# Kernel tuning notes

Hardware: AMD Instinct MI355X
Metric: run time of the kernel (lower is better)

The kernel has to match this reference:

```python
import jax, jax.numpy as jnp
import numpy as np

N, E, D = 20000, 320000, 128


def _glorot(key, shape):
    fan_in, fan_out = shape[0], shape[-1]
    lim = jnp.sqrt(6.0 / (fan_in + fan_out)).astype(jnp.float32)
    return jax.random.uniform(key, shape, jnp.float32, -lim, lim)


def setup_inputs() -> dict:
    key = jax.random.key(0)
    ks = jax.random.split(key, 16)
    h = jax.random.normal(ks[0], (N, 1, D), jnp.float32)
    x = jax.random.normal(ks[1], (N, 3), jnp.float32)
    edge_index = jax.random.randint(ks[2], (2, E), 0, N, jnp.int64)
    # edge_mlp: SPDMLP(2D -> D -> D), 2 linear layers with ReLU between
    W1e = _glorot(ks[3], (2 * D, D)); b1e = jnp.zeros((D,), jnp.float32)
    W2e = _glorot(ks[4], (D, D));     b2e = jnp.zeros((D,), jnp.float32)
    # edge_inf: Linear(D, 1) + Sigmoid
    Wg = _glorot(ks[5], (D, 1));      bg = jnp.zeros((1,), jnp.float32)
    # node_mlp: SPDMLP(2D -> D -> D)
    W1n = _glorot(ks[6], (2 * D, D)); b1n = jnp.zeros((D,), jnp.float32)
    W2n = _glorot(ks[7], (D, D));     b2n = jnp.zeros((D,), jnp.float32)
    return {"h": h, "x": x, "edge_index": edge_index,
            "W1e": W1e, "b1e": b1e, "W2e": W2e, "b2e": b2e,
            "Wg": Wg, "bg": bg,
            "W1n": W1n, "b1n": b1n, "W2n": W2n, "b2n": b2n}


def _feature_joint(a, b):
    # a: [B, Na, Da], b: [B, Nb, Db] -> [B, Na+Nb, Da+Db] block-diagonal concat
    Da, Db = a.shape[2], b.shape[2]
    a_exp = jnp.concatenate([a, jnp.zeros(a.shape[:2] + (Db,), a.dtype)], axis=2)
    b_exp = jnp.concatenate([jnp.zeros(b.shape[:2] + (Da,), b.dtype), b], axis=2)
    return jnp.concatenate([a_exp, b_exp], axis=1)


def _mlp2(y, W1, b1, W2, b2):
    return jax.nn.relu(y @ W1 + b1) @ W2 + b2


def reference(h, x, edge_index, W1e, b1e, W2e, b2e, Wg, bg, W1n, b1n, W2n, b2n):
    src, dst = edge_index[0], edge_index[1]
    hi, hj = h[dst], h[src]                              # [E, 1, D] each
    mij = _mlp2(_feature_joint(hi, hj), W1e, b1e, W2e, b2e)  # [E, 2, D]
    eij = jax.nn.sigmoid(mij @ Wg + bg)                  # [E, 2, 1]
    mi = jax.ops.segment_sum(mij * eij, dst, num_segments=h.shape[0])  # [N, 2, D]
    h_new = h + _mlp2(_feature_joint(mi, h), W1n, b1n, W2n, b2n)       # [N, 3, D]
    return (h_new, x)
```

## Files before the change

### kernel.cpp

```cpp
#include <hip/hip_runtime.h>

#define D    128
#define SP   136
#define FS   132
#define NC   2
#define CAP  64

typedef __attribute__((ext_vector_type(8))) short bf16x8;
typedef __attribute__((ext_vector_type(4))) float f32x4;
typedef unsigned short u16;

__device__ __forceinline__ float sigmoidf(float v) { return 1.0f / (1.0f + __expf(-v)); }

__device__ __forceinline__ u16 f2bf(float x) {
    union { float f; unsigned u; } c; c.f = x;
    return (u16)((c.u + 0x7fffu + ((c.u >> 16) & 1u)) >> 16);
}
__device__ __forceinline__ float bflo(unsigned u) {
    union { unsigned v; float f; } c; c.v = u << 16; return c.f;
}
__device__ __forceinline__ float bfhi(unsigned u) {
    union { unsigned v; float f; } c; c.v = u & 0xffff0000u; return c.f;
}
__device__ __forceinline__ void acc8(float* a, uint4 q) {
    a[0] += bflo(q.x); a[1] += bfhi(q.x);
    a[2] += bflo(q.y); a[3] += bfhi(q.y);
    a[4] += bflo(q.z); a[5] += bfhi(q.z);
    a[6] += bflo(q.w); a[7] += bfhi(q.w);
}

__device__ __forceinline__ void layer32(
    const u16* __restrict__ plane, const short* __restrict__ WbM,
    int lane, int ctbase, f32x4 acc[NC][2])
{
    #pragma unroll
    for (int ks = 0; ks < 4; ++ks) {
        bf16x8 a[2];
        #pragma unroll
        for (int rt = 0; rt < 2; ++rt)
            a[rt] = *reinterpret_cast<const bf16x8*>(
                plane + (rt * 16 + (lane & 15)) * SP + ks * 32 + (lane >> 4) * 8);
        #pragma unroll
        for (int c = 0; c < NC; ++c) {
            const bf16x8 b = *reinterpret_cast<const bf16x8*>(
                WbM + ((ctbase + c) * 4 + ks) * 512 + lane * 8);
            #pragma unroll
            for (int rt = 0; rt < 2; ++rt)
                acc[c][rt] = __builtin_amdgcn_mfma_f32_16x16x32_bf16(a[rt], b, acc[c][rt], 0, 0, 0);
        }
    }
}

__device__ __forceinline__ void store_t32(
    const f32x4 acc[NC][2], const float b1v[NC],
    u16* __restrict__ dst, int lane, int ctbase)
{
    #pragma unroll
    for (int c = 0; c < NC; ++c)
        #pragma unroll
        for (int rt = 0; rt < 2; ++rt)
            #pragma unroll
            for (int rr = 0; rr < 4; ++rr)
                dst[(rt * 16 + (lane >> 4) * 4 + rr) * SP + (ctbase + c) * 16 + (lane & 15)] =
                    f2bf(fmaxf(acc[c][rt][rr] + b1v[c], 0.f));
}

__device__ __forceinline__ void stage32(
    const float* __restrict__ src, int base, int N, int tid, u16* __restrict__ plane)
{
    #pragma unroll
    for (int it = 0; it < 4; ++it) {
        const int idx = it * 256 + tid;
        const int row = idx >> 5, c4 = (idx & 31) << 2;
        int node = base + row; if (node >= N) node = N - 1;
        const float4 v = *reinterpret_cast<const float4*>(&src[(size_t)node * D + c4]);
        ushort4 s;
        s.x = f2bf(v.x); s.y = f2bf(v.y); s.z = f2bf(v.z); s.w = f2bf(v.w);
        *reinterpret_cast<ushort4*>(&plane[row * SP + c4]) = s;
    }
}

__device__ __forceinline__ void mlp_tail(
    const short* __restrict__ Wb, int mA,
    const float* __restrict__ b1n, const float* __restrict__ b2n,
    const float* __restrict__ h, float* __restrict__ out_h,
    int r, int base, int N,
    u16* __restrict__ P1, u16* __restrict__ P2, u16* __restrict__ smem)
{
    const int tid = threadIdx.x, lane = tid & 63, w = tid >> 6;
    const int ctbase = w * NC;

    float b1v[NC], b2v[NC];
    #pragma unroll
    for (int c = 0; c < NC; ++c) {
        const int j = (ctbase + c) * 16 + (lane & 15);
        b1v[c] = b1n[j]; b2v[c] = b2n[j];
    }

    f32x4 acc[NC][2];
    #pragma unroll
    for (int c = 0; c < NC; ++c)
        #pragma unroll
        for (int rt = 0; rt < 2; ++rt) acc[c][rt] = (f32x4){0.f, 0.f, 0.f, 0.f};
    layer32(P1, Wb + (size_t)mA * 16384, lane, ctbase, acc);
    store_t32(acc, b1v, P2, lane, ctbase);
    __syncthreads();

    f32x4 o[NC][2];
    #pragma unroll
    for (int c = 0; c < NC; ++c)
        #pragma unroll
        for (int rt = 0; rt < 2; ++rt) o[c][rt] = (f32x4){0.f, 0.f, 0.f, 0.f};
    layer32(P2, Wb + (size_t)5 * 16384, lane, ctbase, o);
    __syncthreads();

    float* fs = reinterpret_cast<float*>(smem);
    #pragma unroll
    for (int c = 0; c < NC; ++c)
        #pragma unroll
        for (int rt = 0; rt < 2; ++rt)
            #pragma unroll
            for (int rr = 0; rr < 4; ++rr)
                fs[(rt * 16 + (lane >> 4) * 4 + rr) * FS + (ctbase + c) * 16 + (lane & 15)] =
                    o[c][rt][rr] + b2v[c];
    __syncthreads();

    const int nl = tid >> 3, cg = tid & 7;
    const int node = base + nl;
    if (node < N) {
        #pragma unroll
        for (int k = 0; k < 4; ++k) {
            float4 ov = *reinterpret_cast<const float4*>(&fs[nl * FS + cg * 16 + k * 4]);
            const float4 hv = *reinterpret_cast<const float4*>(&h[(size_t)node * D + cg * 16 + k * 4]);
            ov.x += hv.x; ov.y += hv.y; ov.z += hv.z; ov.w += hv.w;
            *reinterpret_cast<float4*>(&out_h[((size_t)node * 3 + r) * D + cg * 16 + k * 4]) = ov;
        }
    }
}

__global__ __launch_bounds__(256) void zero_repack_x_kernel(
    int* __restrict__ cnt, int N, int ZB,
    const float* __restrict__ W1e, const float* __restrict__ W2e,
    const float* __restrict__ W1n, const float* __restrict__ W2n,
    short* __restrict__ Wb,
    const float* __restrict__ x, float* __restrict__ out_x)
{
    const int RB = 48;
    if (blockIdx.x < (unsigned)ZB) {
        const int i = blockIdx.x * 256 + threadIdx.x;
        if (i < N) cnt[i] = 0;
        return;
    }
    if (blockIdx.x >= (unsigned)(ZB + RB)) {
        const int i4 = ((blockIdx.x - ZB - RB) * 256 + threadIdx.x) * 4;
        const int total = N * 3;
        if (i4 + 3 < total) {
            *reinterpret_cast<float4*>(&out_x[i4]) =
                *reinterpret_cast<const float4*>(&x[i4]);
        } else {
            for (int k = i4; k < total && k < i4 + 4; ++k) out_x[k] = x[k];
        }
        return;
    }
    const int gid = (blockIdx.x - ZB) * 256 + threadIdx.x;
    if (gid >= 6 * 8 * 4 * 64) return;
    const int lane = gid & 63;
    int t = gid >> 6;
    const int ks = t & 3; t >>= 2;
    const int ct = t & 7;
    const int m  = t >> 3;
    const float* src;
    switch (m) {
        case 0: src = W1e;             break;
        case 1: src = W1e + 128 * 128; break;
        case 2: src = W2e;             break;
        case 3: src = W1n;             break;
        case 4: src = W1n + 128 * 128; break;
        default: src = W2n;            break;
    }
    const int j  = ct * 16 + (lane & 15);
    const int k0 = ks * 32 + (lane >> 4) * 8;
    bf16x8 hi;
    #pragma unroll
    for (int e = 0; e < 8; ++e) hi[e] = (short)f2bf(src[(size_t)(k0 + e) * 128 + j]);
    *reinterpret_cast<bf16x8*>(Wb + (size_t)m * 16384 + (ct * 4 + ks) * 512 + lane * 8) = hi;
}

__global__ __launch_bounds__(256, 4) void k2_pre_r2_scatter(
    const float* __restrict__ h, const short* __restrict__ Wb,
    const float* __restrict__ b1e, const float* __restrict__ b2e,
    const float* __restrict__ Wg,  const float* __restrict__ bg,
    const float* __restrict__ b1n, const float* __restrict__ b2n,
    u16* __restrict__ Q1b, float* __restrict__ out_h,
    int N, int QB, int MB,
    const int* __restrict__ ei, int E, int* __restrict__ cnt, int* __restrict__ bucket)
{
    __shared__ __align__(16) u16 smem[2 * 32 * SP];
    __shared__ float red_s[4][32];
    u16* P1 = smem;
    u16* P2 = smem + 32 * SP;

    const unsigned bid = blockIdx.x;
    const int tid = threadIdx.x, lane = tid & 63, w = tid >> 6;

    if (bid >= (unsigned)(QB + MB)) {
        const int e = (bid - QB - MB) * 256 + tid;
        if (e < E) {
            const int s = ei[e];
            const int d = ei[E + e];
            const int slot = atomicAdd(&cnt[d], 1);
            if (slot < CAP) bucket[(size_t)d * CAP + slot] = s;
        }
        return;
    }

    if (bid >= (unsigned)QB) {
        const int base = (bid - QB) * 32;
        stage32(h, base, N, tid, P1);
        __syncthreads();
        mlp_tail(Wb, 4, b1n, b2n, h, out_h, 2, base, N, P1, P2, smem);
        return;
    }

    const int base = bid * 32;
    const int ctbase = w * NC;
    stage32(h, base, N, tid, P1);
    __syncthreads();

    float b1v[NC], b2v[NC], wgv[NC];
    #pragma unroll
    for (int c = 0; c < NC; ++c) {
        const int j = (ctbase + c) * 16 + (lane & 15);
        b1v[c] = b1e[j]; b2v[c] = b2e[j]; wgv[c] = Wg[j];
    }
    const float bgv = bg[0];

    f32x4 acc[NC][2];
    #pragma unroll
    for (int c = 0; c < NC; ++c)
        #pragma unroll
        for (int rt = 0; rt < 2; ++rt) acc[c][rt] = (f32x4){0.f, 0.f, 0.f, 0.f};
    layer32(P1, Wb + (size_t)1 * 16384, lane, ctbase, acc);
    store_t32(acc, b1v, P2, lane, ctbase);
    __syncthreads();

    f32x4 p[NC][2];
    #pragma unroll
    for (int c = 0; c < NC; ++c)
        #pragma unroll
        for (int rt = 0; rt < 2; ++rt) p[c][rt] = (f32x4){0.f, 0.f, 0.f, 0.f};
    layer32(P2, Wb + (size_t)2 * 16384, lane, ctbase, p);

    #pragma unroll
    for (int rt = 0; rt < 2; ++rt)
        #pragma unroll
        for (int rr = 0; rr < 4; ++rr) {
            float part = 0.f;
            #pragma unroll
            for (int c = 0; c < NC; ++c) part += (p[c][rt][rr] + b2v[c]) * wgv[c];
            #pragma unroll
            for (int m = 1; m <= 8; m <<= 1) part += __shfl_xor(part, m, 64);
            if ((lane & 15) == 0)
                red_s[w][rt * 16 + (lane >> 4) * 4 + rr] = part;
        }
    __syncthreads();

    #pragma unroll
    for (int rt = 0; rt < 2; ++rt)
        #pragma unroll
        for (int rr = 0; rr < 4; ++rr) {
            const int row = rt * 16 + (lane >> 4) * 4 + rr;
            const float g = sigmoidf(red_s[0][row] + red_s[1][row] +
                                     red_s[2][row] + red_s[3][row] + bgv);
            #pragma unroll
            for (int c = 0; c < NC; ++c)
                P1[row * SP + (ctbase + c) * 16 + (lane & 15)] =
                    f2bf((p[c][rt][rr] + b2v[c]) * g);
        }
    __syncthreads();

    const int nl = tid >> 3, cg = tid & 7;
    const int node = base + nl;
    if (node < N) {
        const uint4 v0 = *reinterpret_cast<const uint4*>(&P1[nl * SP + cg * 16]);
        const uint4 v1 = *reinterpret_cast<const uint4*>(&P1[nl * SP + cg * 16 + 8]);
        *reinterpret_cast<uint4*>(&Q1b[(size_t)node * D + cg * 16])     = v0;
        *reinterpret_cast<uint4*>(&Q1b[(size_t)node * D + cg * 16 + 8]) = v1;
    }
}

__global__ __launch_bounds__(256, 4) void k3_r1_r0(
    const float* __restrict__ h,  const u16* __restrict__ Q1b,
    const short* __restrict__ Wb,
    const float* __restrict__ b1e, const float* __restrict__ b2e,
    const float* __restrict__ Wg,  const float* __restrict__ bg,
    const float* __restrict__ b1n, const float* __restrict__ b2n,
    const int* __restrict__ cnt,  const int* __restrict__ bucket,
    float* __restrict__ out_h, int N, int RT)
{
    __shared__ __align__(16) u16 smem[2 * 32 * SP];
    __shared__ float red_s[4][32];
    u16* P1 = smem;
    u16* P2 = smem + 32 * SP;

    const int tid = threadIdx.x, lane = tid & 63, w = tid >> 6;
    const int ctbase = w * NC;

    if (blockIdx.x < (unsigned)RT) {
        const int base = blockIdx.x * 32;
        const int nl = tid >> 3, cg = tid & 7;
        int node = base + nl; if (node >= N) node = N - 1;
        int deg = cnt[node]; if (deg > CAP) deg = CAP;
        const int* __restrict__ bk = bucket + (size_t)node * CAP;
        const u16* __restrict__ Qc = Q1b + cg * 16;
        float a[16] = {0.f,0.f,0.f,0.f,0.f,0.f,0.f,0.f,0.f,0.f,0.f,0.f,0.f,0.f,0.f,0.f};
        int i = 0;
        for (; i + 1 < deg; i += 2) {
            const int s0 = bk[i], s1 = bk[i + 1];
            const uint4 qa0 = *reinterpret_cast<const uint4*>(Qc + (size_t)s0 * D);
            const uint4 qb0 = *reinterpret_cast<const uint4*>(Qc + (size_t)s0 * D + 8);
            const uint4 qa1 = *reinterpret_cast<const uint4*>(Qc + (size_t)s1 * D);
            const uint4 qb1 = *reinterpret_cast<const uint4*>(Qc + (size_t)s1 * D + 8);
            acc8(a, qa0); acc8(a + 8, qb0);
            acc8(a, qa1); acc8(a + 8, qb1);
        }
        if (i < deg) {
            const int s = bk[i];
            const uint4 qa = *reinterpret_cast<const uint4*>(Qc + (size_t)s * D);
            const uint4 qb = *reinterpret_cast<const uint4*>(Qc + (size_t)s * D + 8);
            acc8(a, qa); acc8(a + 8, qb);
        }
        #pragma unroll
        for (int k4 = 0; k4 < 4; ++k4) {
            ushort4 s4;
            s4.x = f2bf(a[k4 * 4 + 0]); s4.y = f2bf(a[k4 * 4 + 1]);
            s4.z = f2bf(a[k4 * 4 + 2]); s4.w = f2bf(a[k4 * 4 + 3]);
            *reinterpret_cast<ushort4*>(&P1[nl * SP + cg * 16 + k4 * 4]) = s4;
        }
        __syncthreads();
        mlp_tail(Wb, 3, b1n, b2n, h, out_h, 1, base, N, P1, P2, smem);
        return;
    }

    const int base = (blockIdx.x - RT) * 32;
    stage32(h, base, N, tid, P1);
    __syncthreads();

    float b1v[NC], b2v[NC], wgv[NC];
    #pragma unroll
    for (int c = 0; c < NC; ++c) {
        const int j = (ctbase + c) * 16 + (lane & 15);
        b1v[c] = b1e[j]; b2v[c] = b2e[j]; wgv[c] = Wg[j];
    }
    const float bgv = bg[0];

    f32x4 acc[NC][2];
    #pragma unroll
    for (int c = 0; c < NC; ++c)
        #pragma unroll
        for (int rt = 0; rt < 2; ++rt) acc[c][rt] = (f32x4){0.f, 0.f, 0.f, 0.f};
    layer32(P1, Wb, lane, ctbase, acc);
    store_t32(acc, b1v, P2, lane, ctbase);
    __syncthreads();

    f32x4 p[NC][2];
    #pragma unroll
    for (int c = 0; c < NC; ++c)
        #pragma unroll
        for (int rt = 0; rt < 2; ++rt) p[c][rt] = (f32x4){0.f, 0.f, 0.f, 0.f};
    layer32(P2, Wb + (size_t)2 * 16384, lane, ctbase, p);

    #pragma unroll
    for (int rt = 0; rt < 2; ++rt)
        #pragma unroll
        for (int rr = 0; rr < 4; ++rr) {
            float part = 0.f;
            #pragma unroll
            for (int c = 0; c < NC; ++c) part += (p[c][rt][rr] + b2v[c]) * wgv[c];
            #pragma unroll
            for (int m = 1; m <= 8; m <<= 1) part += __shfl_xor(part, m, 64);
            if ((lane & 15) == 0)
                red_s[w][rt * 16 + (lane >> 4) * 4 + rr] = part;
        }
    __syncthreads();

    #pragma unroll
    for (int rt = 0; rt < 2; ++rt)
        #pragma unroll
        for (int rr = 0; rr < 4; ++rr) {
            const int row = rt * 16 + (lane >> 4) * 4 + rr;
            const float g = sigmoidf(red_s[0][row] + red_s[1][row] +
                                     red_s[2][row] + red_s[3][row] + bgv);
            int node2 = base + row; if (node2 >= N) node2 = N - 1;
            const float cv = (float)cnt[node2];
            #pragma unroll
            for (int c = 0; c < NC; ++c)
                P1[row * SP + (ctbase + c) * 16 + (lane & 15)] =
                    f2bf(cv * (p[c][rt][rr] + b2v[c]) * g);
        }
    __syncthreads();
    mlp_tail(Wb, 3, b1n, b2n, h, out_h, 0, base, N, P1, P2, smem);
}

extern "C" void kernel_launch(void* const* d_in, const int* in_sizes, int n_in,
                              void* d_out, int out_size, void* d_ws, size_t ws_size,
                              hipStream_t stream)
{
    const float* h   = (const float*)d_in[0];
    const float* x   = (const float*)d_in[1];
    const int*   ei  = (const int*)d_in[2];
    const float* W1e = (const float*)d_in[3];
    const float* b1e = (const float*)d_in[4];
    const float* W2e = (const float*)d_in[5];
    const float* b2e = (const float*)d_in[6];
    const float* Wg  = (const float*)d_in[7];
    const float* bg  = (const float*)d_in[8];
    const float* W1n = (const float*)d_in[9];
    const float* b1n = (const float*)d_in[10];
    const float* W2n = (const float*)d_in[11];
    const float* b2n = (const float*)d_in[12];

    const int N = in_sizes[0] / D;
    const int E = in_sizes[2] / 2;

    u16*   Q1b    = (u16*)d_ws;
    short* Wb     = (short*)(Q1b + (size_t)N * D);
    int*   cnt    = (int*)(Wb + 6 * 16384);
    int*   bucket = cnt + N;

    float* out_h = (float*)d_out;
    float* out_x = out_h + (size_t)N * 3 * D;

    const int nt = (N + 31) / 32;
    const int ZB = (N + 255) / 256;
    const int RB = 48;
    const int XB = (N * 3 + 1023) / 1024;
    const int QB = nt;
    const int MB = nt;
    const int SB = (E + 255) / 256;

    zero_repack_x_kernel<<<ZB + RB + XB, 256, 0, stream>>>(cnt, N, ZB,
                                                           W1e, W2e, W1n, W2n, Wb, x, out_x);
    k2_pre_r2_scatter<<<QB + MB + SB, 256, 0, stream>>>(h, Wb, b1e, b2e, Wg, bg,
                                                        b1n, b2n, Q1b, out_h,
                                                        N, QB, MB, ei, E, cnt, bucket);
    k3_r1_r0<<<nt * 2, 256, 0, stream>>>(h, Q1b, Wb, b1e, b2e, Wg, bg,
                                         b1n, b2n, cnt, bucket, out_h, N, nt);
}
```

Before: 56.31 us.

## Move row-2 node MLP and x copy into final kernel, coarsen scatter blocks

Moves the independent row-2 node MLP work (h through node MLP) from the middle kernel into the last kernel as extra blocks, and folds the x passthrough copy into those blocks too. The scatter blocks now each process four edges per thread, which cuts the block count. This rebalances work between kernels so the middle kernel, which holds the atomic scatter, is lighter and the final kernel has more blocks to fill the GPU. The risk is a longer tail in the last kernel.

```diff
diff --git a/kernel.cpp b/kernel.cpp
--- a/kernel.cpp
+++ b/kernel.cpp
@@ -138,28 +138,15 @@
     }
 }
 
-__global__ __launch_bounds__(256) void zero_repack_x_kernel(
+__global__ __launch_bounds__(256) void zero_repack_kernel(
     int* __restrict__ cnt, int N, int ZB,
     const float* __restrict__ W1e, const float* __restrict__ W2e,
     const float* __restrict__ W1n, const float* __restrict__ W2n,
-    short* __restrict__ Wb,
-    const float* __restrict__ x, float* __restrict__ out_x)
-{
-    const int RB = 48;
+    short* __restrict__ Wb)
+{
     if (blockIdx.x < (unsigned)ZB) {
         const int i = blockIdx.x * 256 + threadIdx.x;
         if (i < N) cnt[i] = 0;
-        return;
-    }
-    if (blockIdx.x >= (unsigned)(ZB + RB)) {
-        const int i4 = ((blockIdx.x - ZB - RB) * 256 + threadIdx.x) * 4;
-        const int total = N * 3;
-        if (i4 + 3 < total) {
-            *reinterpret_cast<float4*>(&out_x[i4]) =
-                *reinterpret_cast<const float4*>(&x[i4]);
-        } else {
-            for (int k = i4; k < total && k < i4 + 4; ++k) out_x[k] = x[k];
-        }
         return;
     }
     const int gid = (blockIdx.x - ZB) * 256 + threadIdx.x;
@@ -186,13 +173,12 @@
     *reinterpret_cast<bf16x8*>(Wb + (size_t)m * 16384 + (ct * 4 + ks) * 512 + lane * 8) = hi;
 }
 
-__global__ __launch_bounds__(256, 4) void k2_pre_r2_scatter(
+__global__ __launch_bounds__(256, 4) void k2_pre_scatter(
     const float* __restrict__ h, const short* __restrict__ Wb,
     const float* __restrict__ b1e, const float* __restrict__ b2e,
     const float* __restrict__ Wg,  const float* __restrict__ bg,
-    const float* __restrict__ b1n, const float* __restrict__ b2n,
-    u16* __restrict__ Q1b, float* __restrict__ out_h,
-    int N, int QB, int MB,
+    u16* __restrict__ Q1b,
+    int N, int QB,
     const int* __restrict__ ei, int E, int* __restrict__ cnt, int* __restrict__ bucket)
 {
     __shared__ __align__(16) u16 smem[2 * 32 * SP];
@@ -203,22 +189,18 @@
     const unsigned bid = blockIdx.x;
     const int tid = threadIdx.x, lane = tid & 63, w = tid >> 6;
 
-    if (bid >= (unsigned)(QB + MB)) {
-        const int e = (bid - QB - MB) * 256 + tid;
-        if (e < E) {
-            const int s = ei[e];
-            const int d = ei[E + e];
-            const int slot = atomicAdd(&cnt[d], 1);
-            if (slot < CAP) bucket[(size_t)d * CAP + slot] = s;
-        }
-        return;
-    }
-
     if (bid >= (unsigned)QB) {
-        const int base = (bid - QB) * 32;
-        stage32(h, base, N, tid, P1);
-        __syncthreads();
-        mlp_tail(Wb, 4, b1n, b2n, h, out_h, 2, base, N, P1, P2, smem);
+        const int e0 = (bid - QB) * 1024 + tid;
+        #pragma unroll
+        for (int k = 0; k < 4; ++k) {
+            const int e = e0 + k * 256;
+            if (e < E) {
+                const int s = ei[e];
+                const int d = ei[E + e];
+                const int slot = atomicAdd(&cnt[d], 1);
+                if (slot < CAP) bucket[(size_t)d * CAP + slot] = s;
+            }
+        }
         return;
     }
 
@@ -289,13 +271,14 @@
     }
 }
 
-__global__ __launch_bounds__(256, 4) void k3_r1_r0(
+__global__ __launch_bounds__(256, 4) void k3_r1_r0_r2(
     const float* __restrict__ h,  const u16* __restrict__ Q1b,
     const short* __restrict__ Wb,
     const float* __restrict__ b1e, const float* __restrict__ b2e,
     const float* __restrict__ Wg,  const float* __restrict__ bg,
     const float* __restrict__ b1n, const float* __restrict__ b2n,
     const int* __restrict__ cnt,  const int* __restrict__ bucket,
+    const float* __restrict__ x,  float* __restrict__ out_x,
     float* __restrict__ out_h, int N, int RT)
 {
     __shared__ __align__(16) u16 smem[2 * 32 * SP];
@@ -342,6 +325,19 @@
         return;
     }
 
+    if (blockIdx.x >= (unsigned)(2 * RT)) {
+        const int tile = blockIdx.x - 2 * RT;
+        const int base = tile * 32;
+        {
+            const int xi = tile * 96 + tid;
+            if (tid < 96 && xi < N * 3) out_x[xi] = x[xi];
+        }
+        stage32(h, base, N, tid, P1);
+        __syncthreads();
+        mlp_tail(Wb, 4, b1n, b2n, h, out_h, 2, base, N, P1, P2, smem);
+        return;
+    }
+
     const int base = (blockIdx.x - RT) * 32;
     stage32(h, base, N, tid, P1);
     __syncthreads();
@@ -434,16 +430,13 @@
     const int nt = (N + 31) / 32;
     const int ZB = (N + 255) / 256;
     const int RB = 48;
-    const int XB = (N * 3 + 1023) / 1024;
     const int QB = nt;
-    const int MB = nt;
-    const int SB = (E + 255) / 256;
-
-    zero_repack_x_kernel<<<ZB + RB + XB, 256, 0, stream>>>(cnt, N, ZB,
-                                                           W1e, W2e, W1n, W2n, Wb, x, out_x);
-    k2_pre_r2_scatter<<<QB + MB + SB, 256, 0, stream>>>(h, Wb, b1e, b2e, Wg, bg,
-                                                        b1n, b2n, Q1b, out_h,
-                                                        N, QB, MB, ei, E, cnt, bucket);
-    k3_r1_r0<<<nt * 2, 256, 0, stream>>>(h, Q1b, Wb, b1e, b2e, Wg, bg,
-                                         b1n, b2n, cnt, bucket, out_h, N, nt);
-}
+    const int SB = (E + 1023) / 1024;
+
+    zero_repack_kernel<<<ZB + RB, 256, 0, stream>>>(cnt, N, ZB, W1e, W2e, W1n, W2n, Wb);
+    k2_pre_scatter<<<QB + SB, 256, 0, stream>>>(h, Wb, b1e, b2e, Wg, bg, Q1b,
+                                                N, QB, ei, E, cnt, bucket);
+    k3_r1_r0_r2<<<nt * 3, 256, 0, stream>>>(h, Q1b, Wb, b1e, b2e, Wg, bg,
+                                            b1n, b2n, cnt, bucket, x, out_x,
+                                            out_h, N, nt);
+}
```

New measurement: 60.01 us. 1.07x slower.
